# Performance work log

Measured on AMD Instinct MI355X. Metric: run time of the kernel, lower is better.

The kernel has to match this reference:

```python
import jax, jax.numpy as jnp
import numpy as np

# Dims: 3 branches (Temporal/Spatial/Spectral), B batch, C EEG channels, D feat dim
B, C, D, DK, DV, HID, NC, RED = 512, 64, 512, 64, 64, 128, 2, 16
DV3 = 3 * DV
CC = C * C
CCR = CC // RED


def setup_inputs() -> dict:
    key = jax.random.key(0)
    ks = jax.random.split(key, 20)
    f32 = jnp.float32

    def rn(k, shape, s=0.05):
        return jax.random.normal(k, shape, f32) * s

    return {
        "x": jax.random.normal(ks[0], (3, B, C, D), f32),
        "A_init": jax.random.uniform(ks[1], (C, C), f32),
        "dg_fc1_w": rn(ks[2], (3, CC, CCR)), "dg_fc1_b": jnp.zeros((3, CCR), f32),
        "dg_fc2_w": rn(ks[3], (3, CCR, CC)), "dg_fc2_b": jnp.zeros((3, CC), f32),
        "q1_w": rn(ks[4], (3, D, D)), "q1_b": jnp.zeros((3, D), f32),
        "q2_w": rn(ks[5], (3, D, D)), "q2_b": jnp.zeros((3, D), f32),
        "wq_w": rn(ks[6], (3, D, DK)), "wq_b": jnp.zeros((3, DK), f32),
        "wk_w": rn(ks[7], (3, D, DK)), "wk_b": jnp.zeros((3, DK), f32),
        "wv_w": rn(ks[8], (3, D, DV)), "wv_b": jnp.zeros((3, DV), f32),
        "ln_g": jnp.ones((DV3,), f32), "ln_b": jnp.zeros((DV3,), f32),
        "fc1_w": rn(ks[9], (DV3, DV3)), "fc1_b": jnp.zeros((DV3,), f32),
        "fc2_w": rn(ks[10], (DV3, DV3)), "fc2_b": jnp.zeros((DV3,), f32),
        "fm1_w": rn(ks[11], (DV3, DV3)), "fm1_b": jnp.zeros((DV3,), f32),
        "fm2_w": rn(ks[12], (DV3, DV3)), "fm2_b": jnp.zeros((DV3,), f32),
        "out1_w": rn(ks[13], (C * DV3, HID)), "out1_b": jnp.zeros((HID,), f32),
        "out2_w": rn(ks[14], (HID, NC)), "out2_b": jnp.zeros((NC,), f32),
    }


def _forward(x, A_init, dg_fc1_w, dg_fc1_b, dg_fc2_w, dg_fc2_b,
             q1_w, q1_b, q2_w, q2_b, wq_w, wq_b, wk_w, wk_b, wv_w, wv_b,
             ln_g, ln_b, fc1_w, fc1_b, fc2_w, fc2_b, fm1_w, fm1_b,
             fm2_w, fm2_b, out1_w, out1_b, out2_w, out2_b):
    Cn = A_init.shape[0]
    scale = 1.0 / jnp.sqrt(jnp.asarray(DK, x.dtype))

    def branch(xi, f1w, f1b, f2w, f2b, q1w, q1b, q2w, q2b,
               wqw, wqb, wkw, wkb, wvw, wvb):
        # --- DynamicGraphConv: dynamic adjacency from A_init (FC -> ELU -> FC -> ReLU) ---
        A_mid = jax.nn.elu(A_init.reshape(-1) @ f1w + f1b)
        A_dyn = jax.nn.relu(A_mid @ f2w + f2b).reshape(Cn, Cn)
        A_norm = A_dyn / (A_dyn.sum(axis=1, keepdims=True) + 1e-6)  # degree-normalize
        # --- self-gated graph diffusion ---
        h = jax.nn.elu(xi @ q1w + q1b) @ q2w + q2b          # (B,C,D)
        G = jax.nn.elu(jnp.einsum('ij,bjd->bid', A_norm, h) + xi)
        # --- CWTFFNet per-branch channel attention head ---
        Q = G @ wqw + wqb                                    # (B,C,DK)
        K = G @ wkw + wkb
        V = G @ wvw + wvb                                    # (B,C,DV)
        attn = jax.nn.softmax(jnp.einsum('bik,bjk->bij', Q, K) * scale, axis=-1)
        return jnp.einsum('ij,bjv->biv', A_dyn, attn @ V)    # (B,C,DV)

    # vmap over the 3 branches (Temporal/Spatial/Spectral)
    Zs = jax.vmap(branch)(x, dg_fc1_w, dg_fc1_b, dg_fc2_w, dg_fc2_b,
                          q1_w, q1_b, q2_w, q2_b,
                          wq_w, wq_b, wk_w, wk_b, wv_w, wv_b)  # (3,B,C,DV)
    Bn = Zs.shape[1]
    Z_local = jnp.transpose(Zs, (1, 2, 0, 3)).reshape(Bn, Cn, 3 * Zs.shape[-1])  # concat heads
    Z_global = jnp.einsum('ij,bjd->bid', A_init, Z_local)
    cw = jax.nn.softmax(Z_local.mean(axis=1, keepdims=True), axis=-1)  # channel weights
    Zg = Z_global * cw
    # LayerNorm over last dim
    mu = Zg.mean(-1, keepdims=True)
    var = ((Zg - mu) ** 2).mean(-1, keepdims=True)
    Z_ln = (Zg - mu) * jax.lax.rsqrt(var + 1e-5) * ln_g + ln_b
    Z_fc = jax.nn.relu(Z_ln @ fc1_w + fc1_b) @ fc2_w + fc2_b
    Z_fused = Z_fc + (jax.nn.elu(Zg @ fm1_w + fm1_b) @ fm2_w + fm2_b)
    flat = Z_fused.reshape(Bn, -1)
    hdn = jax.nn.relu(flat @ out1_w + out1_b)
    logits = hdn @ out2_w + out2_b
    return logits, Z_fused


def reference(x, A_init, dg_fc1_w, dg_fc1_b, dg_fc2_w, dg_fc2_b,
              q1_w, q1_b, q2_w, q2_b, wq_w, wq_b, wk_w, wk_b, wv_w, wv_b,
              ln_g, ln_b, fc1_w, fc1_b, fc2_w, fc2_b, fm1_w, fm1_b,
              fm2_w, fm2_b, out1_w, out1_b, out2_w, out2_b):
    return _forward(x, A_init, dg_fc1_w, dg_fc1_b, dg_fc2_w, dg_fc2_b,
                    q1_w, q1_b, q2_w, q2_b, wq_w, wq_b, wk_w, wk_b, wv_w, wv_b,
                    ln_g, ln_b, fc1_w, fc1_b, fc2_w, fc2_b, fm1_w, fm1_b,
                    fm2_w, fm2_b, out1_w, out1_b, out2_w, out2_b)
```

## Files before the change

### kernel.cpp

```cpp
#include <hip/hip_runtime.h>
#include <math.h>

typedef unsigned short u16;
typedef __attribute__((ext_vector_type(8))) short short8;
typedef __attribute__((ext_vector_type(4))) float f32x4;
typedef __attribute__((ext_vector_type(4))) unsigned short u16x4;

constexpr int  Bn   = 512;
constexpr int  Cch  = 64;
constexpr int  Dd   = 512;
constexpr int  DV3  = 192;
constexpr long BCD  = (long)Bn * Cch * Dd;
constexpr int  MTOT = Bn * Cch;
constexpr long NZv  = (long)Bn * Cch * DV3;

__device__ __forceinline__ float eluf(float v) { return v > 0.f ? v : expm1f(v); }

__device__ __forceinline__ u16 f2bf(float f) {
  unsigned u = __float_as_uint(f);
  unsigned r = u + 0x7fffu + ((u >> 16) & 1u);
  return (u16)(r >> 16);
}
__device__ __forceinline__ float bf2f(u16 h) { return __uint_as_float(((unsigned)h) << 16); }

typedef __attribute__((address_space(1))) const unsigned int gu32;
typedef __attribute__((address_space(3))) unsigned int lu32;
__device__ __forceinline__ void g2l16(const void* g, void* l) {
  __builtin_amdgcn_global_load_lds((gu32*)g, (lu32*)l, 16, 0, 0);
}

__global__ __launch_bounds__(256) void k_dg1(
    const float* __restrict__ A_init, const float* __restrict__ f1w,
    float* __restrict__ pmid)
{
  int kb = blockIdx.x, z = blockIdx.y, t = threadIdx.x;
  __shared__ float sA[128];
  if (t < 128) sA[t] = A_init[kb * 128 + t];
  __syncthreads();
  const float* w1 = f1w + (long)z * 4096 * 256 + (long)kb * 128 * 256;
  float acc = 0.f;
  #pragma unroll 8
  for (int k = 0; k < 128; ++k) acc = fmaf(sA[k], w1[(long)k * 256 + t], acc);
  pmid[(z * 32 + kb) * 256 + t] = acc;
}

__global__ __launch_bounds__(256) void k_dg2(
    const float* __restrict__ pmid, const float* __restrict__ f1b,
    float* __restrict__ mid)
{
  int z = blockIdx.x, t = threadIdx.x;
  float s = f1b[z * 256 + t];
  #pragma unroll
  for (int kb = 0; kb < 32; ++kb) s += pmid[(z * 32 + kb) * 256 + t];
  mid[z * 256 + t] = eluf(s);
}

__global__ __launch_bounds__(256) void k_dg3(
    const float* __restrict__ mid, const float* __restrict__ f2w,
    const float* __restrict__ f2b,
    float* __restrict__ A_dyn, float* __restrict__ A_norm)
{
  int jb = blockIdx.x, z = blockIdx.y, t = threadIdx.x;
  __shared__ float sM[256];
  sM[t] = mid[z * 256 + t];
  __syncthreads();
  int j = jb * 256 + t;
  const float* w2 = f2w + (long)z * 256 * 4096;
  float acc = f2b[z * 4096 + j];
  #pragma unroll 8
  for (int k = 0; k < 256; ++k) acc = fmaf(sM[k], w2[(long)k * 4096 + j], acc);
  float a = fmaxf(acc, 0.f);
  A_dyn[z * 4096 + j] = a;
  float s = a;
  s += __shfl_xor(s, 1);  s += __shfl_xor(s, 2);  s += __shfl_xor(s, 4);
  s += __shfl_xor(s, 8);  s += __shfl_xor(s, 16); s += __shfl_xor(s, 32);
  A_norm[z * 4096 + j] = a / (s + 1e-6f);
}

__global__ __launch_bounds__(256) void k_cvt_wTh(
    const float* __restrict__ w, u16* __restrict__ hT, int K, int N, int Npad)
{
  int k0 = blockIdx.x * 32, n0 = blockIdx.y * 32, z = blockIdx.z;
  int t = threadIdx.x;
  int tr = t >> 3, tc = (t & 7) * 4;
  long o = (long)z * Npad * K + (long)(n0 + tr) * K + k0 + tc;
  if (n0 >= N) {
    u16x4 zz = {0, 0, 0, 0};
    *(u16x4*)&hT[o] = zz;
    return;
  }
  __shared__ float sT[32][33];
  float4 v = *(const float4*)&w[(long)z * K * N + (long)(k0 + tr) * N + n0 + tc];
  sT[tr][tc + 0] = v.x; sT[tr][tc + 1] = v.y;
  sT[tr][tc + 2] = v.z; sT[tr][tc + 3] = v.w;
  __syncthreads();
  u16x4 h;
  h.x = f2bf(sT[tc + 0][tr]); h.y = f2bf(sT[tc + 1][tr]);
  h.z = f2bf(sT[tc + 2][tr]); h.w = f2bf(sT[tc + 3][tr]);
  *(u16x4*)&hT[o] = h;
}

__global__ __launch_bounds__(256) void k_cvt_qkvTh(
    const float* __restrict__ wq, const float* __restrict__ wk, const float* __restrict__ wv,
    u16* __restrict__ hT)
{
  int k0 = blockIdx.x * 32, n0 = blockIdx.y * 32, z = blockIdx.z;
  int t = threadIdx.x;
  int tr = t >> 3, tc = (t & 7) * 4;
  long o = (long)z * 256 * 512 + (long)(n0 + tr) * 512 + k0 + tc;
  if (n0 >= 192) {
    u16x4 zz = {0, 0, 0, 0};
    *(u16x4*)&hT[o] = zz;
    return;
  }
  const float* src = (n0 < 64) ? wq : (n0 < 128) ? wk : wv;
  int nsub = n0 & 63;
  __shared__ float sT[32][33];
  float4 v = *(const float4*)&src[(long)z * 512 * 64 + (long)(k0 + tr) * 64 + nsub + tc];
  sT[tr][tc + 0] = v.x; sT[tr][tc + 1] = v.y;
  sT[tr][tc + 2] = v.z; sT[tr][tc + 3] = v.w;
  __syncthreads();
  u16x4 h;
  h.x = f2bf(sT[tc + 0][tr]); h.y = f2bf(sT[tc + 1][tr]);
  h.z = f2bf(sT[tc + 2][tr]); h.w = f2bf(sT[tc + 3][tr]);
  *(u16x4*)&hT[o] = h;
}

__global__ __launch_bounds__(256) void k_cvt_qkvb(
    const float* __restrict__ bq, const float* __restrict__ bk, const float* __restrict__ bv,
    float* __restrict__ bcat)
{
  int idx = blockIdx.x * 256 + threadIdx.x;
  if (idx >= 768) return;
  int z = idx >> 8, n = idx & 255;
  float v = 0.f;
  if (n < 64)       v = bq[z * 64 + n];
  else if (n < 128) v = bk[z * 64 + (n - 64)];
  else if (n < 192) v = bv[z * 64 + (n - 128)];
  bcat[idx] = v;
}

template<int ACT, int OMODE, bool AF32, bool RES>
__global__ __launch_bounds__(256) void k_mgemm(
    int N, int K, int lda, int ldo, int Nout,
    const u16* __restrict__ Ah, const u16* __restrict__ Al, long a_zs,
    const u16* __restrict__ Bh, long b_zs,
    const float* __restrict__ bias, long bias_zs,
    float* __restrict__ outF, u16* __restrict__ outH, u16* __restrict__ outL, long o_zs,
    const float* __restrict__ resid)
{
  int gx = gridDim.x, gy = gridDim.y;
  int nwg = gx * gy * (int)gridDim.z;
  int bid = (int)blockIdx.x + gx * ((int)blockIdx.y + gy * (int)blockIdx.z);
  int L = ((nwg & 7) == 0) ? ((bid & 7) * (nwg >> 3) + (bid >> 3)) : bid;
  int n0 = (L % gx) * 128;
  int m0 = ((L / gx) % gy) * 128;
  int z  = L / (gx * gy);

  const u16* ah = Ah + z * a_zs;
  const u16* al = AF32 ? (const u16*)nullptr : (Al + z * a_zs);
  const u16* bh = Bh + z * b_zs;

  __shared__ u16 sm[2][12288];

  int t = threadIdx.x, wv = t >> 6, ln = t & 63;
  int mh = wv >> 1, nh = wv & 1;
  int lr = ln & 15, lk8 = (ln >> 4) * 8;
  f32x4 acc[4][4] = {};

  auto stage = [&](int pp, int kt) {
    u16* smp = sm[pp];
    #pragma unroll
    for (int s = 0; s < 2; ++s) {
      int tile = s * 4 + wv;
      long rowA = (long)(m0 + tile * 16 + lr);
      if (AF32) {
        const float* Af = reinterpret_cast<const float*>(ah);
        const float* g = Af + rowA * lda + kt + lk8;
        g2l16(g,     smp + tile * 1024 + ln * 8);
        g2l16(g + 4, smp + tile * 1024 + 512 + ln * 8);
      } else {
        const u16* gA  = ah + rowA * lda + kt + lk8;
        const u16* gAl = al + rowA * lda + kt + lk8;
        g2l16(gA,  smp + tile * 512 + ln * 8);
        g2l16(gAl, smp + 4096 + tile * 512 + ln * 8);
      }
      const u16* gB = bh + (long)(n0 + tile * 16 + lr) * K + kt + lk8;
      g2l16(gB, smp + 8192 + tile * 512 + ln * 8);
    }
  };

  int nsteps = K >> 5;
  stage(0, 0);
  stage(1, 32);

  for (int it = 0; it < nsteps; ++it) {
    int b = it & 1;
    if (it + 1 < nsteps) { asm volatile("s_waitcnt vmcnt(6)" ::: "memory"); }
    else                 { asm volatile("s_waitcnt vmcnt(0)" ::: "memory"); }
    __builtin_amdgcn_sched_barrier(0);
    __builtin_amdgcn_s_barrier();

    short8 a_h[4], a_l[4], b_h[4];
    if (AF32) {
      const float* fp = reinterpret_cast<const float*>(sm[b]);
      #pragma unroll
      for (int f = 0; f < 4; ++f) {
        f32x4 lo = *(const f32x4*)&fp[(mh * 4 + f) * 512 + ln * 4];
        f32x4 hi = *(const f32x4*)&fp[(mh * 4 + f) * 512 + 256 + ln * 4];
        #pragma unroll
        for (int e = 0; e < 4; ++e) {
          unsigned ul = __float_as_uint(lo[e]), uh = __float_as_uint(hi[e]);
          a_h[f][e]     = (short)(ul >> 16);
          a_h[f][e + 4] = (short)(uh >> 16);
          float rl = lo[e] - __uint_as_float(ul & 0xffff0000u);
          float rh = hi[e] - __uint_as_float(uh & 0xffff0000u);
          a_l[f][e]     = (short)(__float_as_uint(rl) >> 16);
          a_l[f][e + 4] = (short)(__float_as_uint(rh) >> 16);
        }
      }
    } else {
      #pragma unroll
      for (int f = 0; f < 4; ++f) {
        a_h[f] = *(const short8*)&sm[b][(mh * 4 + f) * 512 + ln * 8];
        a_l[f] = *(const short8*)&sm[b][4096 + (mh * 4 + f) * 512 + ln * 8];
      }
    }
    #pragma unroll
    for (int f = 0; f < 4; ++f)
      b_h[f] = *(const short8*)&sm[b][8192 + (nh * 4 + f) * 512 + ln * 8];

    asm volatile("s_waitcnt lgkmcnt(0)" ::: "memory");
    __builtin_amdgcn_sched_barrier(0);
    __builtin_amdgcn_s_barrier();

    if (it + 2 < nsteps) stage(b, (it + 2) << 5);

    __builtin_amdgcn_s_setprio(1);
    #pragma unroll
    for (int i = 0; i < 4; ++i)
      #pragma unroll
      for (int j = 0; j < 4; ++j) {
        acc[i][j] = __builtin_amdgcn_mfma_f32_16x16x32_bf16(a_h[i], b_h[j], acc[i][j], 0, 0, 0);
        acc[i][j] = __builtin_amdgcn_mfma_f32_16x16x32_bf16(a_l[i], b_h[j], acc[i][j], 0, 0, 0);
      }
    __builtin_amdgcn_s_setprio(0);
  }

  int colb = n0 + nh * 64, rowb = m0 + mh * 64;
  #pragma unroll
  for (int i = 0; i < 4; ++i) {
    #pragma unroll
    for (int j = 0; j < 4; ++j) {
      int col = colb + j * 16 + lr;
      if (col < Nout) {
        float bv = bias[z * bias_zs + col];
        #pragma unroll
        for (int r = 0; r < 4; ++r) {
          long row = rowb + i * 16 + (ln >> 4) * 4 + r;
          float v = acc[i][j][r] + bv;
          if (ACT == 1) v = fmaxf(v, 0.f);
          if (ACT == 2) v = eluf(v);
          if (RES) v += resid[z * o_zs + row * ldo + col];
          if (OMODE == 0) {
            outF[z * o_zs + row * ldo + col] = v;
          } else {
            u16 h = f2bf(v);
            outH[z * o_zs + row * ldo + col] = h;
            outL[z * o_zs + row * ldo + col] = f2bf(v - bf2f(h));
          }
        }
      }
    }
  }
}

__global__ __launch_bounds__(256) void k_diffuse(
    const float* __restrict__ A_norm, const u16* __restrict__ Hh,
    const u16* __restrict__ Hl, const float* __restrict__ x,
    u16* __restrict__ Gh, u16* __restrict__ Gl, int b0, int NB)
{
  int b = blockIdx.x, br = blockIdx.y, t = threadIdx.x;
  __shared__ float sAT[64 * 64];
  __shared__ float sH[64 * 64];
  const float* An = A_norm + br * 4096;
  for (int idx = t; idx < 4096; idx += 256)
    sAT[(idx & 63) * 64 + (idx >> 6)] = An[idx];
  const u16* hhb = Hh + ((long)br * NB + b) * (64 * 512);
  const u16* hlb = Hl + ((long)br * NB + b) * (64 * 512);
  const float* xb = x + ((long)br * Bn + (b0 + b)) * (64 * 512);
  u16* Ghb = Gh + ((long)br * NB + b) * (64 * 512);
  u16* Glb = Gl + ((long)br * NB + b) * (64 * 512);
  int c4 = t & 15, rb = (t >> 4) * 4;
  for (int dc = 0; dc < 512; dc += 64) {
    __syncthreads();
    for (int idx = t * 4; idx < 4096; idx += 1024) {
      int r = idx >> 6, c = idx & 63;
      long off = (long)r * 512 + dc + c;
      u16x4 ha = *(const u16x4*)&hhb[off];
      u16x4 la = *(const u16x4*)&hlb[off];
      sH[idx + 0] = bf2f(ha.x) + bf2f(la.x);
      sH[idx + 1] = bf2f(ha.y) + bf2f(la.y);
      sH[idx + 2] = bf2f(ha.z) + bf2f(la.z);
      sH[idx + 3] = bf2f(ha.w) + bf2f(la.w);
    }
    __syncthreads();
    float acc[4][4] = {};
    #pragma unroll 4
    for (int j = 0; j < 64; ++j) {
      float a0 = sAT[j * 64 + rb + 0], a1 = sAT[j * 64 + rb + 1];
      float a2 = sAT[j * 64 + rb + 2], a3 = sAT[j * 64 + rb + 3];
      float4 hv = *(const float4*)&sH[j * 64 + c4 * 4];
      acc[0][0] = fmaf(a0, hv.x, acc[0][0]); acc[0][1] = fmaf(a0, hv.y, acc[0][1]);
      acc[0][2] = fmaf(a0, hv.z, acc[0][2]); acc[0][3] = fmaf(a0, hv.w, acc[0][3]);
      acc[1][0] = fmaf(a1, hv.x, acc[1][0]); acc[1][1] = fmaf(a1, hv.y, acc[1][1]);
      acc[1][2] = fmaf(a1, hv.z, acc[1][2]); acc[1][3] = fmaf(a1, hv.w, acc[1][3]);
      acc[2][0] = fmaf(a2, hv.x, acc[2][0]); acc[2][1] = fmaf(a2, hv.y, acc[2][1]);
      acc[2][2] = fmaf(a2, hv.z, acc[2][2]); acc[2][3] = fmaf(a2, hv.w, acc[2][3]);
      acc[3][0] = fmaf(a3, hv.x, acc[3][0]); acc[3][1] = fmaf(a3, hv.y, acc[3][1]);
      acc[3][2] = fmaf(a3, hv.z, acc[3][2]); acc[3][3] = fmaf(a3, hv.w, acc[3][3]);
    }
    #pragma unroll
    for (int i = 0; i < 4; ++i) {
      float4 xv = *(const float4*)&xb[(long)(rb + i) * 512 + dc + c4 * 4];
      float v0 = eluf(acc[i][0] + xv.x);
      float v1 = eluf(acc[i][1] + xv.y);
      float v2 = eluf(acc[i][2] + xv.z);
      float v3 = eluf(acc[i][3] + xv.w);
      u16x4 hh, ll;
      hh.x = f2bf(v0); ll.x = f2bf(v0 - bf2f(hh.x));
      hh.y = f2bf(v1); ll.y = f2bf(v1 - bf2f(hh.y));
      hh.z = f2bf(v2); ll.z = f2bf(v2 - bf2f(hh.z));
      hh.w = f2bf(v3); ll.w = f2bf(v3 - bf2f(hh.w));
      long o = (long)(rb + i) * 512 + dc + c4 * 4;
      *(u16x4*)&Ghb[o] = hh;
      *(u16x4*)&Glb[o] = ll;
    }
  }
}

__global__ __launch_bounds__(256) void k_attn(
    const float* __restrict__ qkv, const float* __restrict__ A_dyn,
    float* __restrict__ Zl, int b0, int NB)
{
  int b = blockIdx.x, br = blockIdx.y, t = threadIdx.x;
  __shared__ float sQ[64 * 65];
  __shared__ float sK[64 * 65];
  __shared__ float sS[64 * 65];
  const float* Qb = qkv + ((long)br * NB + b) * (64 * 256);
  for (int idx = t * 4; idx < 4096; idx += 1024) {
    int r = idx >> 6, c = idx & 63;
    float4 q4 = *(const float4*)&Qb[(long)r * 256 + c];
    float4 k4 = *(const float4*)&Qb[(long)r * 256 + 64 + c];
    sQ[r * 65 + c + 0] = q4.x; sQ[r * 65 + c + 1] = q4.y;
    sQ[r * 65 + c + 2] = q4.z; sQ[r * 65 + c + 3] = q4.w;
    sK[r * 65 + c + 0] = k4.x; sK[r * 65 + c + 1] = k4.y;
    sK[r * 65 + c + 2] = k4.z; sK[r * 65 + c + 3] = k4.w;
  }
  __syncthreads();
  int c4 = t & 15, rb = (t >> 4) * 4;
  float acc[4][4] = {};
  #pragma unroll 4
  for (int k = 0; k < 64; ++k) {
    float a0 = sQ[(rb + 0) * 65 + k], a1 = sQ[(rb + 1) * 65 + k];
    float a2 = sQ[(rb + 2) * 65 + k], a3 = sQ[(rb + 3) * 65 + k];
    #pragma unroll
    for (int q = 0; q < 4; ++q) {
      float bq = sK[(c4 * 4 + q) * 65 + k];
      acc[0][q] = fmaf(a0, bq, acc[0][q]); acc[1][q] = fmaf(a1, bq, acc[1][q]);
      acc[2][q] = fmaf(a2, bq, acc[2][q]); acc[3][q] = fmaf(a3, bq, acc[3][q]);
    }
  }
  #pragma unroll
  for (int i = 0; i < 4; ++i)
    #pragma unroll
    for (int q = 0; q < 4; ++q)
      sS[(rb + i) * 65 + c4 * 4 + q] = acc[i][q] * 0.125f;
  __syncthreads();
  {
    int r = t >> 2, l = t & 3;
    float m = -3.4e38f;
    #pragma unroll
    for (int c = 0; c < 16; ++c) m = fmaxf(m, sS[r * 65 + l * 16 + c]);
    m = fmaxf(m, __shfl_xor(m, 1));
    m = fmaxf(m, __shfl_xor(m, 2));
    float s = 0.f, e[16];
    #pragma unroll
    for (int c = 0; c < 16; ++c) { e[c] = expf(sS[r * 65 + l * 16 + c] - m); s += e[c]; }
    s += __shfl_xor(s, 1);
    s += __shfl_xor(s, 2);
    float inv = 1.f / s;
    #pragma unroll
    for (int c = 0; c < 16; ++c) sS[r * 65 + l * 16 + c] = e[c] * inv;
  }
  __syncthreads();
  for (int idx = t * 4; idx < 4096; idx += 1024) {
    int r = idx >> 6, c = idx & 63;
    float4 v4 = *(const float4*)&Qb[(long)r * 256 + 128 + c];
    sQ[r * 65 + c + 0] = v4.x; sQ[r * 65 + c + 1] = v4.y;
    sQ[r * 65 + c + 2] = v4.z; sQ[r * 65 + c + 3] = v4.w;
  }
  __syncthreads();
  float pv[4][4] = {};
  #pragma unroll 4
  for (int j = 0; j < 64; ++j) {
    float p0 = sS[(rb + 0) * 65 + j], p1 = sS[(rb + 1) * 65 + j];
    float p2 = sS[(rb + 2) * 65 + j], p3 = sS[(rb + 3) * 65 + j];
    #pragma unroll
    for (int q = 0; q < 4; ++q) {
      float vq = sQ[j * 65 + c4 * 4 + q];
      pv[0][q] = fmaf(p0, vq, pv[0][q]); pv[1][q] = fmaf(p1, vq, pv[1][q]);
      pv[2][q] = fmaf(p2, vq, pv[2][q]); pv[3][q] = fmaf(p3, vq, pv[3][q]);
    }
  }
  #pragma unroll
  for (int i = 0; i < 4; ++i)
    #pragma unroll
    for (int q = 0; q < 4; ++q)
      sK[(rb + i) * 65 + c4 * 4 + q] = pv[i][q];
  __syncthreads();
  const float* Ad = A_dyn + br * 4096;
  for (int idx = t; idx < 4096; idx += 256)
    sS[(idx >> 6) * 65 + (idx & 63)] = Ad[idx];
  __syncthreads();
  float zz[4][4] = {};
  #pragma unroll 4
  for (int j = 0; j < 64; ++j) {
    float a0 = sS[(rb + 0) * 65 + j], a1 = sS[(rb + 1) * 65 + j];
    float a2 = sS[(rb + 2) * 65 + j], a3 = sS[(rb + 3) * 65 + j];
    #pragma unroll
    for (int q = 0; q < 4; ++q) {
      float p = sK[j * 65 + c4 * 4 + q];
      zz[0][q] = fmaf(a0, p, zz[0][q]); zz[1][q] = fmaf(a1, p, zz[1][q]);
      zz[2][q] = fmaf(a2, p, zz[2][q]); zz[3][q] = fmaf(a3, p, zz[3][q]);
    }
  }
  long zbase = ((long)(b0 + b) * 64) * 192 + br * 64;
  #pragma unroll
  for (int i = 0; i < 4; ++i) {
    float4 o; o.x = zz[i][0]; o.y = zz[i][1]; o.z = zz[i][2]; o.w = zz[i][3];
    *(float4*)&Zl[zbase + (long)(rb + i) * 192 + c4 * 4] = o;
  }
}

template<int ACT, bool RES, bool SPLITK>
__global__ __launch_bounds__(256) void k_gemm(
    int M, int N, int K,
    const float* __restrict__ A, long a_zs, int lda,
    const float* __restrict__ W, long w_zs,
    const float* __restrict__ bias, long b_zs,
    float* __restrict__ out, long o_zs,
    const float* __restrict__ resid, int k_chunk)
{
  int z  = blockIdx.z;
  int n0 = blockIdx.x * 64, m0 = blockIdx.y * 64;
  const float* Ab = A + (SPLITK ? 0 : z * a_zs);
  const float* Wb = W + (SPLITK ? 0 : z * w_zs);
  float* ob = out + z * o_zs;
  const float* bb = bias ? bias + z * b_zs : nullptr;
  const float* rb_ = RES ? resid + z * o_zs : nullptr;
  int k0   = SPLITK ? z * k_chunk : 0;
  int kend = SPLITK ? k0 + k_chunk : K;

  __shared__ float As[16][68];
  __shared__ float Bs[16][68];
  float acc[4][4] = {};
  int t  = threadIdx.x;
  int tm = t & 15, tn = t >> 4;
  int ar = t >> 2, ak = (t & 3) * 4;
  int bk = t >> 4, bn = (t & 15) * 4;

  for (int kt = k0; kt < kend; kt += 16) {
    float4 av = *(const float4*)&Ab[(long)(m0 + ar) * lda + kt + ak];
    float4 bv = *(const float4*)&Wb[(long)(kt + bk) * N + n0 + bn];
    __syncthreads();
    As[ak + 0][ar] = av.x; As[ak + 1][ar] = av.y;
    As[ak + 2][ar] = av.z; As[ak + 3][ar] = av.w;
    *(float4*)&Bs[bk][bn] = bv;
    __syncthreads();
    #pragma unroll
    for (int k = 0; k < 16; ++k) {
      float4 a = *(const float4*)&As[k][tm * 4];
      float4 b = *(const float4*)&Bs[k][tn * 4];
      acc[0][0] = fmaf(a.x, b.x, acc[0][0]); acc[0][1] = fmaf(a.x, b.y, acc[0][1]);
      acc[0][2] = fmaf(a.x, b.z, acc[0][2]); acc[0][3] = fmaf(a.x, b.w, acc[0][3]);
      acc[1][0] = fmaf(a.y, b.x, acc[1][0]); acc[1][1] = fmaf(a.y, b.y, acc[1][1]);
      acc[1][2] = fmaf(a.y, b.z, acc[1][2]); acc[1][3] = fmaf(a.y, b.w, acc[1][3]);
      acc[2][0] = fmaf(a.z, b.x, acc[2][0]); acc[2][1] = fmaf(a.z, b.y, acc[2][1]);
      acc[2][2] = fmaf(a.z, b.z, acc[2][2]); acc[2][3] = fmaf(a.z, b.w, acc[2][3]);
      acc[3][0] = fmaf(a.w, b.x, acc[3][0]); acc[3][1] = fmaf(a.w, b.y, acc[3][1]);
      acc[3][2] = fmaf(a.w, b.z, acc[3][2]); acc[3][3] = fmaf(a.w, b.w, acc[3][3]);
    }
  }

  #pragma unroll
  for (int i = 0; i < 4; ++i) {
    long row = m0 + tm * 4 + i;
    int  col = n0 + tn * 4;
    float v[4];
    #pragma unroll
    for (int j = 0; j < 4; ++j) {
      float x = acc[i][j] + (bb ? bb[col + j] : 0.f);
      if (ACT == 1) x = fmaxf(x, 0.f);
      if (ACT == 2) x = eluf(x);
      v[j] = x;
    }
    if (RES) {
      float4 r = *(const float4*)&rb_[row * N + col];
      v[0] += r.x; v[1] += r.y; v[2] += r.z; v[3] += r.w;
    }
    float4 o; o.x = v[0]; o.y = v[1]; o.z = v[2]; o.w = v[3];
    *(float4*)&ob[row * N + col] = o;
  }
}

__global__ __launch_bounds__(256) void k_fuse(
    const float* __restrict__ Zl, const float* __restrict__ A_init,
    const float* __restrict__ ln_g, const float* __restrict__ ln_b,
    u16* __restrict__ ZgH, u16* __restrict__ ZgL,
    u16* __restrict__ ZlnH, u16* __restrict__ ZlnL)
{
  int b = blockIdx.x, t = threadIdx.x;
  __shared__ float sZ[64 * 192];
  __shared__ float sAT[64 * 64];
  const float* Zb = Zl + (long)b * 64 * 192;
  for (int idx = t * 4; idx < 12288; idx += 1024)
    *(float4*)&sZ[idx] = *(const float4*)&Zb[idx];
  __syncthreads();
  if (t < 192) {
    float s = 0.f;
    #pragma unroll 8
    for (int j = 0; j < 64; ++j) s += sZ[j * 192 + t];
    sAT[t] = s * (1.f / 64.f);
  }
  __syncthreads();
  float m = -3.4e38f;
  for (int d = 0; d < 192; ++d) m = fmaxf(m, sAT[d]);
  float ssum = 0.f;
  for (int d = 0; d < 192; ++d) ssum += expf(sAT[d] - m);
  float cinv = 1.f / ssum;
  int c4 = t & 15, rb = (t >> 4) * 4;
  float cw[12];
  #pragma unroll
  for (int cc = 0; cc < 3; ++cc)
    #pragma unroll
    for (int q = 0; q < 4; ++q)
      cw[cc * 4 + q] = expf(sAT[cc * 64 + c4 * 4 + q] - m) * cinv;
  __syncthreads();
  for (int idx = t; idx < 4096; idx += 256)
    sAT[(idx & 63) * 64 + (idx >> 6)] = A_init[idx];
  __syncthreads();
  float acc[3][4][4] = {};
  for (int j = 0; j < 64; ++j) {
    float a0 = sAT[j * 64 + rb + 0], a1 = sAT[j * 64 + rb + 1];
    float a2 = sAT[j * 64 + rb + 2], a3 = sAT[j * 64 + rb + 3];
    #pragma unroll
    for (int cc = 0; cc < 3; ++cc) {
      float4 zv = *(const float4*)&sZ[j * 192 + cc * 64 + c4 * 4];
      acc[cc][0][0] = fmaf(a0, zv.x, acc[cc][0][0]); acc[cc][0][1] = fmaf(a0, zv.y, acc[cc][0][1]);
      acc[cc][0][2] = fmaf(a0, zv.z, acc[cc][0][2]); acc[cc][0][3] = fmaf(a0, zv.w, acc[cc][0][3]);
      acc[cc][1][0] = fmaf(a1, zv.x, acc[cc][1][0]); acc[cc][1][1] = fmaf(a1, zv.y, acc[cc][1][1]);
      acc[cc][1][2] = fmaf(a1, zv.z, acc[cc][1][2]); acc[cc][1][3] = fmaf(a1, zv.w, acc[cc][1][3]);
      acc[cc][2][0] = fmaf(a2, zv.x, acc[cc][2][0]); acc[cc][2][1] = fmaf(a2, zv.y, acc[cc][2][1]);
      acc[cc][2][2] = fmaf(a2, zv.z, acc[cc][2][2]); acc[cc][2][3] = fmaf(a2, zv.w, acc[cc][2][3]);
      acc[cc][3][0] = fmaf(a3, zv.x, acc[cc][3][0]); acc[cc][3][1] = fmaf(a3, zv.y, acc[cc][3][1]);
      acc[cc][3][2] = fmaf(a3, zv.z, acc[cc][3][2]); acc[cc][3][3] = fmaf(a3, zv.w, acc[cc][3][3]);
    }
  }
  long obase = (long)b * 64 * 192;
  #pragma unroll
  for (int cc = 0; cc < 3; ++cc)
    #pragma unroll
    for (int i = 0; i < 4; ++i)
      #pragma unroll
      for (int q = 0; q < 4; ++q)
        acc[cc][i][q] *= cw[cc * 4 + q];
  #pragma unroll
  for (int cc = 0; cc < 3; ++cc)
    #pragma unroll
    for (int i = 0; i < 4; ++i) {
      u16x4 hh, ll;
      hh.x = f2bf(acc[cc][i][0]); ll.x = f2bf(acc[cc][i][0] - bf2f(hh.x));
      hh.y = f2bf(acc[cc][i][1]); ll.y = f2bf(acc[cc][i][1] - bf2f(hh.y));
      hh.z = f2bf(acc[cc][i][2]); ll.z = f2bf(acc[cc][i][2] - bf2f(hh.z));
      hh.w = f2bf(acc[cc][i][3]); ll.w = f2bf(acc[cc][i][3] - bf2f(hh.w));
      long o = obase + (long)(rb + i) * 192 + cc * 64 + c4 * 4;
      *(u16x4*)&ZgH[o] = hh;
      *(u16x4*)&ZgL[o] = ll;
    }
  __syncthreads();
  #pragma unroll
  for (int cc = 0; cc < 3; ++cc)
    #pragma unroll
    for (int i = 0; i < 4; ++i) {
      float4 o; o.x = acc[cc][i][0]; o.y = acc[cc][i][1]; o.z = acc[cc][i][2]; o.w = acc[cc][i][3];
      *(float4*)&sZ[(rb + i) * 192 + cc * 64 + c4 * 4] = o;
    }
  __syncthreads();
  {
    int r = t >> 2, l = t & 3;
    float s = 0.f, s2 = 0.f;
    for (int ci = 0; ci < 48; ++ci) {
      int c = ci + r; if (c >= 48) c -= 48;
      float v = sZ[r * 192 + l * 48 + c];
      s += v; s2 = fmaf(v, v, s2);
    }
    s  += __shfl_xor(s, 1);  s  += __shfl_xor(s, 2);
    s2 += __shfl_xor(s2, 1); s2 += __shfl_xor(s2, 2);
    float mu = s * (1.f / 192.f);
    float var = s2 * (1.f / 192.f) - mu * mu;
    float rstd = rsqrtf(var + 1e-5f);
    for (int ci = 0; ci < 48; ++ci) {
      int c = ci + r; if (c >= 48) c -= 48;
      int d = l * 48 + c;
      float v = sZ[r * 192 + d];
      float o = (v - mu) * rstd * ln_g[d] + ln_b[d];
      u16 h = f2bf(o);
      ZlnH[obase + (long)r * 192 + d] = h;
      ZlnL[obase + (long)r * 192 + d] = f2bf(o - bf2f(h));
    }
  }
}

__global__ __launch_bounds__(128) void k_final(
    const float* __restrict__ partial, const float* __restrict__ o1b,
    const float* __restrict__ o2w, const float* __restrict__ o2b,
    float* __restrict__ logits, int nsplit)
{
  int b = blockIdx.x, t = threadIdx.x;
  __shared__ float sH[128];
  float a = o1b[t];
  for (int s = 0; s < nsplit; ++s) a += partial[(long)s * 512 * 128 + b * 128 + t];
  a = fmaxf(a, 0.f);
  sH[t] = a;
  __syncthreads();
  if (t < 2) {
    float z = o2b[t];
    #pragma unroll 8
    for (int h = 0; h < 128; ++h) z = fmaf(sH[h], o2w[h * 2 + t], z);
    logits[b * 2 + t] = z;
  }
}

extern "C" void kernel_launch(void* const* d_in, const int* in_sizes, int n_in,
                              void* d_out, int out_size, void* d_ws, size_t ws_size,
                              hipStream_t stream)
{
  const float* x      = (const float*)d_in[0];
  const float* A_init = (const float*)d_in[1];
  const float* f1w = (const float*)d_in[2];
  const float* f1b = (const float*)d_in[3];
  const float* f2w = (const float*)d_in[4];
  const float* f2b = (const float*)d_in[5];
  const float* q1w = (const float*)d_in[6];
  const float* q1b = (const float*)d_in[7];
  const float* q2w = (const float*)d_in[8];
  const float* q2b = (const float*)d_in[9];
  const float* wqw = (const float*)d_in[10];
  const float* wqb = (const float*)d_in[11];
  const float* wkw = (const float*)d_in[12];
  const float* wkb = (const float*)d_in[13];
  const float* wvw = (const float*)d_in[14];
  const float* wvb = (const float*)d_in[15];
  const float* lng = (const float*)d_in[16];
  const float* lnb = (const float*)d_in[17];
  const float* fc1w = (const float*)d_in[18];
  const float* fc1b = (const float*)d_in[19];
  const float* fc2w = (const float*)d_in[20];
  const float* fc2b = (const float*)d_in[21];
  const float* fm1w = (const float*)d_in[22];
  const float* fm1b = (const float*)d_in[23];
  const float* fm2w = (const float*)d_in[24];
  const float* fm2b = (const float*)d_in[25];
  const float* o1w  = (const float*)d_in[26];
  const float* o1b  = (const float*)d_in[27];
  const float* o2w  = (const float*)d_in[28];
  const float* o2b  = (const float*)d_in[29];

  float* outF   = (float*)d_out;
  float* logits = outF;
  float* Zfused = outF + 1024;

  size_t off = 0;
  char* base = (char*)d_ws;
  auto alloc = [&](size_t bytes) -> void* {
    void* p = base + off;
    off += (bytes + 255) & ~(size_t)255;
    return p;
  };
  float* A_dyn  = (float*)alloc(3 * 4096 * 4);
  float* A_norm = (float*)alloc(3 * 4096 * 4);
  float* pmid   = (float*)alloc(3 * 32 * 256 * 4);
  float* mid    = (float*)alloc(3 * 256 * 4);
  u16* q1T_h  = (u16*)alloc((size_t)3 * 512 * 512 * 2);
  u16* q2T_h  = (u16*)alloc((size_t)3 * 512 * 512 * 2);
  u16* qkvT_h = (u16*)alloc((size_t)3 * 256 * 512 * 2);
  float* qkvb = (float*)alloc(3 * 256 * 4);
  u16* fc1T_h = (u16*)alloc(256 * 192 * 2);
  u16* fc2T_h = (u16*)alloc(256 * 192 * 2);
  u16* fm1T_h = (u16*)alloc(256 * 192 * 2);
  u16* fm2T_h = (u16*)alloc(256 * 192 * 2);
  float* Zl  = (float*)alloc(NZv * 4);
  u16* ZgH  = (u16*)alloc(NZv * 2); u16* ZgL  = (u16*)alloc(NZv * 2);
  u16* ZlnH = (u16*)alloc(NZv * 2); u16* ZlnL = (u16*)alloc(NZv * 2);
  u16* tmH  = (u16*)alloc(NZv * 2); u16* tmL  = (u16*)alloc(NZv * 2);
  float* s2f = (float*)alloc(NZv * 4);
  float* partial = (float*)alloc((size_t)24 * 512 * 128 * 4);

  int NB = 512;
  while (NB > 32) {
    if (off + (size_t)NB * 786432ULL + 65536 <= ws_size) break;
    NB >>= 1;
  }
  long CM  = (long)NB * 64;
  long an  = (long)NB * 32768;
  u16* th = (u16*)alloc((size_t)3 * an * 2);
  u16* tl = (u16*)alloc((size_t)3 * an * 2);
  u16* hh = (u16*)alloc((size_t)3 * an * 2);
  u16* hl = (u16*)alloc((size_t)3 * an * 2);
  float* qkvB = (float*)hh;

  k_dg1<<<dim3(32, 3), 256, 0, stream>>>(A_init, f1w, pmid);
  k_dg2<<<dim3(3), 256, 0, stream>>>(pmid, f1b, mid);
  k_dg3<<<dim3(16, 3), 256, 0, stream>>>(mid, f2w, f2b, A_dyn, A_norm);
  k_cvt_wTh<<<dim3(16, 16, 3), 256, 0, stream>>>(q1w, q1T_h, 512, 512, 512);
  k_cvt_wTh<<<dim3(16, 16, 3), 256, 0, stream>>>(q2w, q2T_h, 512, 512, 512);
  k_cvt_qkvTh<<<dim3(16, 8, 3), 256, 0, stream>>>(wqw, wkw, wvw, qkvT_h);
  k_cvt_qkvb<<<dim3(3), 256, 0, stream>>>(wqb, wkb, wvb, qkvb);
  k_cvt_wTh<<<dim3(6, 8, 1), 256, 0, stream>>>(fc1w, fc1T_h, 192, 192, 256);
  k_cvt_wTh<<<dim3(6, 8, 1), 256, 0, stream>>>(fc2w, fc2T_h, 192, 192, 256);
  k_cvt_wTh<<<dim3(6, 8, 1), 256, 0, stream>>>(fm1w, fm1T_h, 192, 192, 256);
  k_cvt_wTh<<<dim3(6, 8, 1), 256, 0, stream>>>(fm2w, fm2T_h, 192, 192, 256);

  for (int b0 = 0; b0 < Bn; b0 += NB) {
    const float* xc = x + (long)b0 * 64 * 512;
    k_mgemm<2, 1, true, false><<<dim3(4, (unsigned)(NB / 2), 3), 256, 0, stream>>>(
        512, 512, 512, 512, 512,
        (const u16*)xc, nullptr, BCD * 2, q1T_h, (long)512 * 512,
        q1b, 512, nullptr, th, tl, an, nullptr);
    k_mgemm<0, 1, false, false><<<dim3(4, (unsigned)(NB / 2), 3), 256, 0, stream>>>(
        512, 512, 512, 512, 512,
        th, tl, an, q2T_h, (long)512 * 512,
        q2b, 512, nullptr, hh, hl, an, nullptr);
    k_diffuse<<<dim3(NB, 3), 256, 0, stream>>>(A_norm, hh, hl, x, th, tl, b0, NB);
    k_mgemm<0, 0, false, false><<<dim3(2, (unsigned)(NB / 2), 3), 256, 0, stream>>>(
        256, 512, 512, 256, 192,
        th, tl, an, qkvT_h, (long)256 * 512,
        qkvb, 256, qkvB, nullptr, nullptr, CM * 256, nullptr);
    k_attn<<<dim3(NB, 3), 256, 0, stream>>>(qkvB, A_dyn, Zl, b0, NB);
  }

  k_fuse<<<dim3(Bn), 256, 0, stream>>>(Zl, A_init, lng, lnb, ZgH, ZgL, ZlnH, ZlnL);
  k_mgemm<1, 1, false, false><<<dim3(2, 256, 1), 256, 0, stream>>>(
      256, 192, 192, 192, 192,
      ZlnH, ZlnL, 0, fc1T_h, 0, fc1b, 0, nullptr, tmH, tmL, 0, nullptr);
  k_mgemm<0, 0, false, false><<<dim3(2, 256, 1), 256, 0, stream>>>(
      256, 192, 192, 192, 192,
      tmH, tmL, 0, fc2T_h, 0, fc2b, 0, s2f, nullptr, nullptr, 0, nullptr);
  k_mgemm<2, 1, false, false><<<dim3(2, 256, 1), 256, 0, stream>>>(
      256, 192, 192, 192, 192,
      ZgH, ZgL, 0, fm1T_h, 0, fm1b, 0, nullptr, tmH, tmL, 0, nullptr);
  k_mgemm<0, 0, false, true><<<dim3(2, 256, 1), 256, 0, stream>>>(
      256, 192, 192, 192, 192,
      tmH, tmL, 0, fm2T_h, 0, fm2b, 0, Zfused, nullptr, nullptr, 0, s2f);
  k_gemm<0, false, true><<<dim3(2, 8, 24), 256, 0, stream>>>(
      512, 128, 12288, Zfused, 0, 12288, o1w, 0, nullptr, 0,
      partial, (long)512 * 128, nullptr, 512);
  k_final<<<dim3(512), 128, 0, stream>>>(partial, o1b, o2w, o2b, logits, 24);
}
```

Measured before the change: 1.176 ms.

## Split channel-weight softmax into its own kernel and shrink fuse kernel LDS

Channel-weight softmax moves into a separate small kernel, so the fuse kernel no longer stages the full 64x192 Z tile in shared memory. The fuse kernel instead processes the three 64-column slices in turn through a padded 64x68 LDS buffer. It computes LayerNorm statistics from registers via warp shuffles rather than a second shared-memory pass, and writes LN outputs vectorised. The aim is lower LDS use for better occupancy and fewer scalar stores, at the cost of an extra launch and a second read of Zl.

Result: faster. 1.128 ms (-4.1%).

```diff
diff --git a/kernel.cpp b/kernel.cpp
--- a/kernel.cpp
+++ b/kernel.cpp
@@ -514,110 +514,118 @@
   }
 }
 
-__global__ __launch_bounds__(256) void k_fuse(
+__global__ __launch_bounds__(192) void k_cw(
+    const float* __restrict__ Zl, float* __restrict__ cw)
+{
+  int b = blockIdx.x, t = threadIdx.x;
+  __shared__ float sM[192];
+  const float* Zb = Zl + (long)b * 12288;
+  float s = 0.f;
+  #pragma unroll 8
+  for (int j = 0; j < 64; ++j) s += Zb[j * 192 + t];
+  sM[t] = s * (1.f / 64.f);
+  __syncthreads();
+  float m = -3.4e38f;
+  for (int d = 0; d < 192; ++d) m = fmaxf(m, sM[d]);
+  float ss = 0.f;
+  for (int d = 0; d < 192; ++d) ss += expf(sM[d] - m);
+  cw[b * 192 + t] = expf(sM[t] - m) / ss;
+}
+
+__global__ __launch_bounds__(256) void k_fuse2(
     const float* __restrict__ Zl, const float* __restrict__ A_init,
+    const float* __restrict__ cw,
     const float* __restrict__ ln_g, const float* __restrict__ ln_b,
     u16* __restrict__ ZgH, u16* __restrict__ ZgL,
     u16* __restrict__ ZlnH, u16* __restrict__ ZlnL)
 {
   int b = blockIdx.x, t = threadIdx.x;
-  __shared__ float sZ[64 * 192];
   __shared__ float sAT[64 * 64];
-  const float* Zb = Zl + (long)b * 64 * 192;
-  for (int idx = t * 4; idx < 12288; idx += 1024)
-    *(float4*)&sZ[idx] = *(const float4*)&Zb[idx];
-  __syncthreads();
-  if (t < 192) {
-    float s = 0.f;
-    #pragma unroll 8
-    for (int j = 0; j < 64; ++j) s += sZ[j * 192 + t];
-    sAT[t] = s * (1.f / 64.f);
-  }
-  __syncthreads();
-  float m = -3.4e38f;
-  for (int d = 0; d < 192; ++d) m = fmaxf(m, sAT[d]);
-  float ssum = 0.f;
-  for (int d = 0; d < 192; ++d) ssum += expf(sAT[d] - m);
-  float cinv = 1.f / ssum;
-  int c4 = t & 15, rb = (t >> 4) * 4;
-  float cw[12];
-  #pragma unroll
-  for (int cc = 0; cc < 3; ++cc)
-    #pragma unroll
-    for (int q = 0; q < 4; ++q)
-      cw[cc * 4 + q] = expf(sAT[cc * 64 + c4 * 4 + q] - m) * cinv;
-  __syncthreads();
+  __shared__ float sH[64 * 68];
   for (int idx = t; idx < 4096; idx += 256)
     sAT[(idx & 63) * 64 + (idx >> 6)] = A_init[idx];
-  __syncthreads();
-  float acc[3][4][4] = {};
-  for (int j = 0; j < 64; ++j) {
-    float a0 = sAT[j * 64 + rb + 0], a1 = sAT[j * 64 + rb + 1];
-    float a2 = sAT[j * 64 + rb + 2], a3 = sAT[j * 64 + rb + 3];
-    #pragma unroll
-    for (int cc = 0; cc < 3; ++cc) {
-      float4 zv = *(const float4*)&sZ[j * 192 + cc * 64 + c4 * 4];
-      acc[cc][0][0] = fmaf(a0, zv.x, acc[cc][0][0]); acc[cc][0][1] = fmaf(a0, zv.y, acc[cc][0][1]);
-      acc[cc][0][2] = fmaf(a0, zv.z, acc[cc][0][2]); acc[cc][0][3] = fmaf(a0, zv.w, acc[cc][0][3]);
-      acc[cc][1][0] = fmaf(a1, zv.x, acc[cc][1][0]); acc[cc][1][1] = fmaf(a1, zv.y, acc[cc][1][1]);
-      acc[cc][1][2] = fmaf(a1, zv.z, acc[cc][1][2]); acc[cc][1][3] = fmaf(a1, zv.w, acc[cc][1][3]);
-      acc[cc][2][0] = fmaf(a2, zv.x, acc[cc][2][0]); acc[cc][2][1] = fmaf(a2, zv.y, acc[cc][2][1]);
-      acc[cc][2][2] = fmaf(a2, zv.z, acc[cc][2][2]); acc[cc][2][3] = fmaf(a2, zv.w, acc[cc][2][3]);
-      acc[cc][3][0] = fmaf(a3, zv.x, acc[cc][3][0]); acc[cc][3][1] = fmaf(a3, zv.y, acc[cc][3][1]);
-      acc[cc][3][2] = fmaf(a3, zv.z, acc[cc][3][2]); acc[cc][3][3] = fmaf(a3, zv.w, acc[cc][3][3]);
-    }
-  }
-  long obase = (long)b * 64 * 192;
-  #pragma unroll
-  for (int cc = 0; cc < 3; ++cc)
-    #pragma unroll
-    for (int i = 0; i < 4; ++i)
-      #pragma unroll
-      for (int q = 0; q < 4; ++q)
-        acc[cc][i][q] *= cw[cc * 4 + q];
-  #pragma unroll
-  for (int cc = 0; cc < 3; ++cc)
+  const float* Zb = Zl + (long)b * 12288;
+  long obase = (long)b * 12288;
+  int c4 = t & 15, rb = (t >> 4) * 4;
+  float zg[3][4][4];
+  float rs[4] = {0.f, 0.f, 0.f, 0.f};
+  float rs2[4] = {0.f, 0.f, 0.f, 0.f};
+
+  #pragma unroll
+  for (int cc = 0; cc < 3; ++cc) {
+    __syncthreads();
+    for (int idx = t * 4; idx < 4096; idx += 1024) {
+      int r = idx >> 6, c = idx & 63;
+      float4 v = *(const float4*)&Zb[(long)r * 192 + cc * 64 + c];
+      *(float4*)&sH[r * 68 + c] = v;
+    }
+    __syncthreads();
+    float acc[4][4] = {};
+    #pragma unroll 4
+    for (int j = 0; j < 64; ++j) {
+      float a0 = sAT[j * 64 + rb + 0], a1 = sAT[j * 64 + rb + 1];
+      float a2 = sAT[j * 64 + rb + 2], a3 = sAT[j * 64 + rb + 3];
+      float4 hv = *(const float4*)&sH[j * 68 + c4 * 4];
+      acc[0][0] = fmaf(a0, hv.x, acc[0][0]); acc[0][1] = fmaf(a0, hv.y, acc[0][1]);
+      acc[0][2] = fmaf(a0, hv.z, acc[0][2]); acc[0][3] = fmaf(a0, hv.w, acc[0][3]);
+      acc[1][0] = fmaf(a1, hv.x, acc[1][0]); acc[1][1] = fmaf(a1, hv.y, acc[1][1]);
+      acc[1][2] = fmaf(a1, hv.z, acc[1][2]); acc[1][3] = fmaf(a1, hv.w, acc[1][3]);
+      acc[2][0] = fmaf(a2, hv.x, acc[2][0]); acc[2][1] = fmaf(a2, hv.y, acc[2][1]);
+      acc[2][2] = fmaf(a2, hv.z, acc[2][2]); acc[2][3] = fmaf(a2, hv.w, acc[2][3]);
+      acc[3][0] = fmaf(a3, hv.x, acc[3][0]); acc[3][1] = fmaf(a3, hv.y, acc[3][1]);
+      acc[3][2] = fmaf(a3, hv.z, acc[3][2]); acc[3][3] = fmaf(a3, hv.w, acc[3][3]);
+    }
+    float4 cwv = *(const float4*)&cw[b * 192 + cc * 64 + c4 * 4];
     #pragma unroll
     for (int i = 0; i < 4; ++i) {
+      float v0 = acc[i][0] * cwv.x;
+      float v1 = acc[i][1] * cwv.y;
+      float v2 = acc[i][2] * cwv.z;
+      float v3 = acc[i][3] * cwv.w;
+      zg[cc][i][0] = v0; zg[cc][i][1] = v1; zg[cc][i][2] = v2; zg[cc][i][3] = v3;
+      rs[i]  += v0 + v1 + v2 + v3;
+      rs2[i] += v0 * v0 + v1 * v1 + v2 * v2 + v3 * v3;
       u16x4 hh, ll;
-      hh.x = f2bf(acc[cc][i][0]); ll.x = f2bf(acc[cc][i][0] - bf2f(hh.x));
-      hh.y = f2bf(acc[cc][i][1]); ll.y = f2bf(acc[cc][i][1] - bf2f(hh.y));
-      hh.z = f2bf(acc[cc][i][2]); ll.z = f2bf(acc[cc][i][2] - bf2f(hh.z));
-      hh.w = f2bf(acc[cc][i][3]); ll.w = f2bf(acc[cc][i][3] - bf2f(hh.w));
+      hh.x = f2bf(v0); ll.x = f2bf(v0 - bf2f(hh.x));
+      hh.y = f2bf(v1); ll.y = f2bf(v1 - bf2f(hh.y));
+      hh.z = f2bf(v2); ll.z = f2bf(v2 - bf2f(hh.z));
+      hh.w = f2bf(v3); ll.w = f2bf(v3 - bf2f(hh.w));
       long o = obase + (long)(rb + i) * 192 + cc * 64 + c4 * 4;
       *(u16x4*)&ZgH[o] = hh;
       *(u16x4*)&ZgL[o] = ll;
     }
-  __syncthreads();
-  #pragma unroll
-  for (int cc = 0; cc < 3; ++cc)
+  }
+
+  #pragma unroll
+  for (int i = 0; i < 4; ++i) {
+    float s = rs[i], s2 = rs2[i];
+    s  += __shfl_xor(s, 1);  s  += __shfl_xor(s, 2);
+    s  += __shfl_xor(s, 4);  s  += __shfl_xor(s, 8);
+    s2 += __shfl_xor(s2, 1); s2 += __shfl_xor(s2, 2);
+    s2 += __shfl_xor(s2, 4); s2 += __shfl_xor(s2, 8);
+    rs[i] = s; rs2[i] = s2;
+  }
+  #pragma unroll
+  for (int cc = 0; cc < 3; ++cc) {
+    float4 g4 = *(const float4*)&ln_g[cc * 64 + c4 * 4];
+    float4 b4 = *(const float4*)&ln_b[cc * 64 + c4 * 4];
     #pragma unroll
     for (int i = 0; i < 4; ++i) {
-      float4 o; o.x = acc[cc][i][0]; o.y = acc[cc][i][1]; o.z = acc[cc][i][2]; o.w = acc[cc][i][3];
-      *(float4*)&sZ[(rb + i) * 192 + cc * 64 + c4 * 4] = o;
-    }
-  __syncthreads();
-  {
-    int r = t >> 2, l = t & 3;
-    float s = 0.f, s2 = 0.f;
-    for (int ci = 0; ci < 48; ++ci) {
-      int c = ci + r; if (c >= 48) c -= 48;
-      float v = sZ[r * 192 + l * 48 + c];
-      s += v; s2 = fmaf(v, v, s2);
-    }
-    s  += __shfl_xor(s, 1);  s  += __shfl_xor(s, 2);
-    s2 += __shfl_xor(s2, 1); s2 += __shfl_xor(s2, 2);
-    float mu = s * (1.f / 192.f);
-    float var = s2 * (1.f / 192.f) - mu * mu;
-    float rstd = rsqrtf(var + 1e-5f);
-    for (int ci = 0; ci < 48; ++ci) {
-      int c = ci + r; if (c >= 48) c -= 48;
-      int d = l * 48 + c;
-      float v = sZ[r * 192 + d];
-      float o = (v - mu) * rstd * ln_g[d] + ln_b[d];
-      u16 h = f2bf(o);
-      ZlnH[obase + (long)r * 192 + d] = h;
-      ZlnL[obase + (long)r * 192 + d] = f2bf(o - bf2f(h));
+      float mu  = rs[i] * (1.f / 192.f);
+      float var = rs2[i] * (1.f / 192.f) - mu * mu;
+      float rstd = rsqrtf(var + 1e-5f);
+      float v0 = (zg[cc][i][0] - mu) * rstd * g4.x + b4.x;
+      float v1 = (zg[cc][i][1] - mu) * rstd * g4.y + b4.y;
+      float v2 = (zg[cc][i][2] - mu) * rstd * g4.z + b4.z;
+      float v3 = (zg[cc][i][3] - mu) * rstd * g4.w + b4.w;
+      u16x4 hh, ll;
+      hh.x = f2bf(v0); ll.x = f2bf(v0 - bf2f(hh.x));
+      hh.y = f2bf(v1); ll.y = f2bf(v1 - bf2f(hh.y));
+      hh.z = f2bf(v2); ll.z = f2bf(v2 - bf2f(hh.z));
+      hh.w = f2bf(v3); ll.w = f2bf(v3 - bf2f(hh.w));
+      long o = obase + (long)(rb + i) * 192 + cc * 64 + c4 * 4;
+      *(u16x4*)&ZlnH[o] = hh;
+      *(u16x4*)&ZlnL[o] = ll;
     }
   }
 }
@@ -701,6 +709,7 @@
   u16* fm1T_h = (u16*)alloc(256 * 192 * 2);
   u16* fm2T_h = (u16*)alloc(256 * 192 * 2);
   float* Zl  = (float*)alloc(NZv * 4);
+  float* cwB = (float*)alloc((size_t)Bn * 192 * 4);
   u16* ZgH  = (u16*)alloc(NZv * 2); u16* ZgL  = (u16*)alloc(NZv * 2);
   u16* ZlnH = (u16*)alloc(NZv * 2); u16* ZlnL = (u16*)alloc(NZv * 2);
   u16* tmH  = (u16*)alloc(NZv * 2); u16* tmL  = (u16*)alloc(NZv * 2);
@@ -750,7 +759,8 @@
     k_attn<<<dim3(NB, 3), 256, 0, stream>>>(qkvB, A_dyn, Zl, b0, NB);
   }
 
-  k_fuse<<<dim3(Bn), 256, 0, stream>>>(Zl, A_init, lng, lnb, ZgH, ZgL, ZlnH, ZlnL);
+  k_cw<<<dim3(Bn), 192, 0, stream>>>(Zl, cwB);
+  k_fuse2<<<dim3(Bn), 256, 0, stream>>>(Zl, A_init, cwB, lng, lnb, ZgH, ZgL, ZlnH, ZlnL);
   k_mgemm<1, 1, false, false><<<dim3(2, 256, 1), 256, 0, stream>>>(
       256, 192, 192, 192, 192,
       ZlnH, ZlnL, 0, fc1T_h, 0, fc1b, 0, nullptr, tmH, tmL, 0, nullptr);
```
